# Optimization experiments

Measured on AMD Instinct MI355X. Metric: run time of the kernel, lower is better.

Reference implementation:

```python
import jax, jax.numpy as jnp
import numpy as np

T, C, O, N = 131072, 512, 512, 1024


def setup_inputs() -> dict:
    key = jax.random.key(0)
    k1, k2, k3, k4, k5 = jax.random.split(key, 5)
    x = jax.random.normal(k1, (T, C), dtype=jnp.float32)
    segment_ids = jnp.sort(jax.random.randint(k2, (T,), 0, N)).astype(jnp.int64)
    # proj_func: Linear(C, O); score_func: Linear(C, 1)
    Wp = jax.random.normal(k3, (C, O), dtype=jnp.float32) / np.sqrt(C)
    bp = jnp.zeros((O,), dtype=jnp.float32)
    ws = jax.random.normal(k4, (C,), dtype=jnp.float32) / np.sqrt(C)
    bs = jnp.zeros((), dtype=jnp.float32)
    return {"x": x, "Wp": Wp, "bp": bp, "ws": ws, "bs": bs,
            "segment_ids": segment_ids, "num_segments": N}


def reference(x, Wp, bp, ws, bs, segment_ids, num_segments):
    # proj_x = Linear(x): [T, O]
    proj_x = x @ Wp + bp
    # score = Linear(x) squeezed to [T]
    score = x @ ws + bs
    # segment-wise numerically stable softmax over ragged segments
    seg_max = jax.ops.segment_max(score, segment_ids, num_segments=num_segments)
    seg_max = jnp.where(jnp.isfinite(seg_max), seg_max, 0.0)  # empty segments
    e = jnp.exp(score - seg_max[segment_ids])
    denom = jax.ops.segment_sum(e, segment_ids, num_segments=num_segments)
    w = e / denom[segment_ids]  # [T]
    # per-segment weighted sum of projected features -> [N, O]
    out = jax.ops.segment_sum(proj_x * w[:, None], segment_ids,
                              num_segments=num_segments)
    return out
```

## Files before the change

### kernel.cpp

```cpp
#include <hip/hip_runtime.h>
#include <hip/hip_bf16.h>
#include <cstdint>
#include <cstddef>

#define CC 512
#define OO 512
#define NN 1024
#define QP 4

typedef float f4 __attribute__((ext_vector_type(4)));

__global__ void seg_bounds_kernel(const int* __restrict__ sid,
                                  int* __restrict__ seg_start,
                                  int T, int N) {
    int t = blockIdx.x * blockDim.x + threadIdx.x;
    if (t >= T) return;
    int s  = sid[t];
    int sp = (t == 0) ? -1 : sid[t - 1];
    for (int n = sp + 1; n <= s; ++n) seg_start[n] = t;
    if (t == T - 1) {
        for (int n = s + 1; n <= N; ++n) seg_start[n] = T;
    }
}

__device__ __forceinline__ float dot4(const f4 a, const f4 b) {
    return a.x * b.x + a.y * b.y + a.z * b.z + a.w * b.w;
}

__device__ __forceinline__ float wave_sum(float p) {
    #pragma unroll
    for (int off = 32; off >= 1; off >>= 1)
        p += __shfl_xor(p, off, 64);
    return p;
}

__global__ __launch_bounds__(64) void seg_pool_partial(
    const float* __restrict__ x,
    const float* __restrict__ ws_g,
    const float* __restrict__ bs_g,
    const int*   __restrict__ seg_start,
    float*       __restrict__ pacc,
    float*       __restrict__ pl)
{
    const int g = blockIdx.x;
    const int n = g >> 2;
    const int q = g & 3;
    const int s = seg_start[n];
    const int e = seg_start[n + 1];
    const int len = e - s;
    const int tb = s + (((len * q) >> 2) & ~7);
    const int te = (q == 3) ? e : (s + (((len * (q + 1)) >> 2) & ~7));
    const int lane = threadIdx.x;
    const int c0 = lane * 4;

    const f4 w0 = *reinterpret_cast<const f4*>(ws_g + c0);
    const f4 w1 = *reinterpret_cast<const f4*>(ws_g + 256 + c0);
    const float bsv = bs_g[0];

    float l = 0.f;
    f4 a0 = {0.f, 0.f, 0.f, 0.f};
    f4 a1 = {0.f, 0.f, 0.f, 0.f};

    const int nCh   = (te - tb) >> 2;
    const int start = ((g & 7) * nCh) >> 3;

    f4 A0[4], A1[4], B0[4], B1[4];

    auto PTR = [&](int i) {
        int idx = start + i;
        idx = (idx >= nCh) ? (idx - nCh) : idx;
        return x + (size_t)(tb + idx * 4) * CC;
    };

    auto LOAD4 = [&](f4 (&b0)[4], f4 (&b1)[4], const float* p) {
        #pragma unroll
        for (int j = 0; j < 4; ++j) {
            const float* r = p + (size_t)j * CC;
            b0[j] = __builtin_nontemporal_load(reinterpret_cast<const f4*>(r + c0));
            b1[j] = __builtin_nontemporal_load(reinterpret_cast<const f4*>(r + 256 + c0));
        }
    };

    auto COMP4 = [&](const f4 (&b0)[4], const f4 (&b1)[4]) {
        float sc[4];
        #pragma unroll
        for (int j = 0; j < 4; ++j)
            sc[j] = wave_sum(dot4(b0[j], w0) + dot4(b1[j], w1)) + bsv;
        #pragma unroll
        for (int j = 0; j < 4; ++j) {
            const float wj = __expf(sc[j]);
            l += wj;
            a0 += wj * b0[j];
            a1 += wj * b1[j];
        }
    };

    if (nCh > 0) {
        LOAD4(A0, A1, PTR(0));
        int i = 0;
        for (; i + 1 < nCh; i += 2) {
            LOAD4(B0, B1, PTR(i + 1));
            COMP4(A0, A1);
            if (i + 2 < nCh) LOAD4(A0, A1, PTR(i + 2));
            COMP4(B0, B1);
        }
        if (nCh & 1) COMP4(A0, A1);
    }

    for (int t0 = tb + nCh * 4; t0 < te; t0 += 4) {
        #pragma unroll
        for (int j = 0; j < 4; ++j) {
            int t = t0 + j;
            t = (t < te) ? t : (te - 1);
            const float* r = x + (size_t)t * CC;
            A0[j] = __builtin_nontemporal_load(reinterpret_cast<const f4*>(r + c0));
            A1[j] = __builtin_nontemporal_load(reinterpret_cast<const f4*>(r + 256 + c0));
        }
        #pragma unroll
        for (int j = 0; j < 4; ++j) {
            float sc = wave_sum(dot4(A0[j], w0) + dot4(A1[j], w1)) + bsv;
            if (t0 + j >= te) sc = -INFINITY;
            const float wj = __expf(sc);
            l += wj;
            a0 += wj * A0[j];
            a1 += wj * A1[j];
        }
    }

    float* pa = pacc + (size_t)g * CC;
    *reinterpret_cast<f4*>(pa + c0)       = a0;
    *reinterpret_cast<f4*>(pa + 256 + c0) = a1;
    if (lane == 0) pl[g] = l;
}

__global__ __launch_bounds__(64) void seg_combine(
    const float* __restrict__ pacc,
    const float* __restrict__ pl,
    float*       __restrict__ y)
{
    const int n = blockIdx.x;
    const int lane = threadIdx.x;
    const int c0 = lane * 4;

    float L = 0.f;
    f4 o0 = {0.f, 0.f, 0.f, 0.f};
    f4 o1 = {0.f, 0.f, 0.f, 0.f};
    #pragma unroll
    for (int q = 0; q < QP; ++q) {
        L += pl[n * QP + q];
        const float* pa = pacc + (size_t)(n * QP + q) * CC;
        o0 += *reinterpret_cast<const f4*>(pa + c0);
        o1 += *reinterpret_cast<const f4*>(pa + 256 + c0);
    }
    const float inv = (L > 0.f) ? (1.f / L) : 0.f;
    o0 *= inv;
    o1 *= inv;
    float* yp = y + (size_t)n * CC;
    *reinterpret_cast<f4*>(yp + c0)       = o0;
    *reinterpret_cast<f4*>(yp + 256 + c0) = o1;
}

__global__ __launch_bounds__(256) void proj_kernel(
    float*       __restrict__ out,
    const float* __restrict__ Wp,
    const float* __restrict__ bp,
    const int*   __restrict__ seg_start)
{
    const int n0  = blockIdx.x * 4;
    const int tid = threadIdx.x;

    __shared__ float ylds[4][CC];
    {
        const float* src = out + (size_t)n0 * CC;
        for (int idx = tid; idx < 4 * CC / 4; idx += 256)
            reinterpret_cast<f4*>(&ylds[0][0])[idx] =
                reinterpret_cast<const f4*>(src)[idx];
    }
    __syncthreads();

    const int o0 = tid;
    const int o1 = tid + 256;
    float acc[4][2] = {};

    for (int k = 0; k < CC; k += 4) {
        f4 yv[4];
        #pragma unroll
        for (int r = 0; r < 4; ++r)
            yv[r] = *reinterpret_cast<const f4*>(&ylds[r][k]);
        #pragma unroll
        for (int kk = 0; kk < 4; ++kk) {
            const float w0 = Wp[(size_t)(k + kk) * OO + o0];
            const float w1 = Wp[(size_t)(k + kk) * OO + o1];
            #pragma unroll
            for (int r = 0; r < 4; ++r) {
                const float yval = (kk == 0) ? yv[r].x :
                                   (kk == 1) ? yv[r].y :
                                   (kk == 2) ? yv[r].z : yv[r].w;
                acc[r][0] += yval * w0;
                acc[r][1] += yval * w1;
            }
        }
    }

    #pragma unroll
    for (int r = 0; r < 4; ++r) {
        const int n = n0 + r;
        const bool nonempty = seg_start[n + 1] > seg_start[n];
        const float b0 = nonempty ? bp[o0] : 0.f;
        const float b1 = nonempty ? bp[o1] : 0.f;
        out[(size_t)n * OO + o0] = acc[r][0] + b0;
        out[(size_t)n * OO + o1] = acc[r][1] + b1;
    }
}

extern "C" void kernel_launch(void* const* d_in, const int* in_sizes, int n_in,
                              void* d_out, int out_size, void* d_ws, size_t ws_size,
                              hipStream_t stream) {
    const float* x    = (const float*)d_in[0];
    const float* Wp   = (const float*)d_in[1];
    const float* bp   = (const float*)d_in[2];
    const float* wsv  = (const float*)d_in[3];
    const float* bs   = (const float*)d_in[4];
    const int*   sid  = (const int*)d_in[5];
    const int T = in_sizes[5];
    const int N = NN;

    int*   seg_start = (int*)d_ws;
    float* pacc      = (float*)((char*)d_ws + 8192);
    float* pl        = (float*)((char*)d_ws + 8192 +
                                (size_t)N * QP * CC * sizeof(float));
    float* out       = (float*)d_out;

    seg_bounds_kernel<<<(T + 255) / 256, 256, 0, stream>>>(sid, seg_start, T, N);
    seg_pool_partial<<<N * QP, 64, 0, stream>>>(x, wsv, bs, seg_start, pacc, pl);
    seg_combine<<<N, 64, 0, stream>>>(pacc, pl, out);
    proj_kernel<<<N / 4, 256, 0, stream>>>(out, Wp, bp, seg_start);
}
```

Before: 89.25 us.

## Fuse partial combine into projection GEMM and simplify pooling pipeline

Merges the separate combine kernel into the projection kernel: each 512-thread block sums the four partial accumulators for 8 segments into LDS, applies the 1/L normalisation after the matmul, and writes the output directly. This drops one launch and the intermediate write and read of the pooled features. The pooling loop is restructured into sequential 8-row A/B double buffering, the rotated start offset is removed, and nontemporal loads become plain loads. The projection tile also changes from 4 segments x 2 outputs per thread to 8 segments x 1 output per thread. Possible costs are lower occupancy from 512-thread blocks and fewer blocks (128) in the projection stage.

```diff
diff --git a/kernel.cpp b/kernel.cpp
--- a/kernel.cpp
+++ b/kernel.cpp
@@ -7,6 +7,7 @@
 #define OO 512
 #define NN 1024
 #define QP 4
+#define RB 8
 
 typedef float f4 __attribute__((ext_vector_type(4)));
 
@@ -61,60 +62,78 @@
     f4 a0 = {0.f, 0.f, 0.f, 0.f};
     f4 a1 = {0.f, 0.f, 0.f, 0.f};
 
-    const int nCh   = (te - tb) >> 2;
-    const int start = ((g & 7) * nCh) >> 3;
+    const int nPair = (te - tb) >> 3;
 
     f4 A0[4], A1[4], B0[4], B1[4];
 
-    auto PTR = [&](int i) {
-        int idx = start + i;
-        idx = (idx >= nCh) ? (idx - nCh) : idx;
-        return x + (size_t)(tb + idx * 4) * CC;
-    };
-
-    auto LOAD4 = [&](f4 (&b0)[4], f4 (&b1)[4], const float* p) {
+    auto LOAD4A = [&](const float* p) {
         #pragma unroll
         for (int j = 0; j < 4; ++j) {
             const float* r = p + (size_t)j * CC;
-            b0[j] = __builtin_nontemporal_load(reinterpret_cast<const f4*>(r + c0));
-            b1[j] = __builtin_nontemporal_load(reinterpret_cast<const f4*>(r + 256 + c0));
-        }
-    };
-
-    auto COMP4 = [&](const f4 (&b0)[4], const f4 (&b1)[4]) {
+            A0[j] = *reinterpret_cast<const f4*>(r + c0);
+            A1[j] = *reinterpret_cast<const f4*>(r + 256 + c0);
+        }
+    };
+    auto LOAD4B = [&](const float* p) {
+        #pragma unroll
+        for (int j = 0; j < 4; ++j) {
+            const float* r = p + (size_t)j * CC;
+            B0[j] = *reinterpret_cast<const f4*>(r + c0);
+            B1[j] = *reinterpret_cast<const f4*>(r + 256 + c0);
+        }
+    };
+
+    auto COMP4A = [&]() {
         float sc[4];
         #pragma unroll
         for (int j = 0; j < 4; ++j)
-            sc[j] = wave_sum(dot4(b0[j], w0) + dot4(b1[j], w1)) + bsv;
+            sc[j] = wave_sum(dot4(A0[j], w0) + dot4(A1[j], w1)) + bsv;
         #pragma unroll
         for (int j = 0; j < 4; ++j) {
             const float wj = __expf(sc[j]);
             l += wj;
-            a0 += wj * b0[j];
-            a1 += wj * b1[j];
-        }
-    };
-
-    if (nCh > 0) {
-        LOAD4(A0, A1, PTR(0));
-        int i = 0;
-        for (; i + 1 < nCh; i += 2) {
-            LOAD4(B0, B1, PTR(i + 1));
-            COMP4(A0, A1);
-            if (i + 2 < nCh) LOAD4(A0, A1, PTR(i + 2));
-            COMP4(B0, B1);
-        }
-        if (nCh & 1) COMP4(A0, A1);
-    }
-
-    for (int t0 = tb + nCh * 4; t0 < te; t0 += 4) {
+            a0 += wj * A0[j];
+            a1 += wj * A1[j];
+        }
+    };
+    auto COMP4B = [&]() {
+        float sc[4];
+        #pragma unroll
+        for (int j = 0; j < 4; ++j)
+            sc[j] = wave_sum(dot4(B0[j], w0) + dot4(B1[j], w1)) + bsv;
+        #pragma unroll
+        for (int j = 0; j < 4; ++j) {
+            const float wj = __expf(sc[j]);
+            l += wj;
+            a0 += wj * B0[j];
+            a1 += wj * B1[j];
+        }
+    };
+
+    const float* base = x + (size_t)tb * CC;
+
+    if (nPair >= 1) {
+        LOAD4A(base);
+        LOAD4B(base + 4 * CC);
+        for (int p = 0; p < nPair - 1; ++p) {
+            const float* nxt = base + (size_t)(p * 8 + 8) * CC;
+            COMP4A();
+            LOAD4A(nxt);
+            COMP4B();
+            LOAD4B(nxt + 4 * CC);
+        }
+        COMP4A();
+        COMP4B();
+    }
+
+    for (int t0 = tb + nPair * 8; t0 < te; t0 += 4) {
         #pragma unroll
         for (int j = 0; j < 4; ++j) {
             int t = t0 + j;
             t = (t < te) ? t : (te - 1);
             const float* r = x + (size_t)t * CC;
-            A0[j] = __builtin_nontemporal_load(reinterpret_cast<const f4*>(r + c0));
-            A1[j] = __builtin_nontemporal_load(reinterpret_cast<const f4*>(r + 256 + c0));
+            A0[j] = *reinterpret_cast<const f4*>(r + c0);
+            A1[j] = *reinterpret_cast<const f4*>(r + 256 + c0);
         }
         #pragma unroll
         for (int j = 0; j < 4; ++j) {
@@ -133,83 +152,58 @@
     if (lane == 0) pl[g] = l;
 }
 
-__global__ __launch_bounds__(64) void seg_combine(
+__global__ __launch_bounds__(512) void proj_combine(
     const float* __restrict__ pacc,
     const float* __restrict__ pl,
-    float*       __restrict__ y)
-{
-    const int n = blockIdx.x;
-    const int lane = threadIdx.x;
-    const int c0 = lane * 4;
-
-    float L = 0.f;
-    f4 o0 = {0.f, 0.f, 0.f, 0.f};
-    f4 o1 = {0.f, 0.f, 0.f, 0.f};
-    #pragma unroll
-    for (int q = 0; q < QP; ++q) {
-        L += pl[n * QP + q];
-        const float* pa = pacc + (size_t)(n * QP + q) * CC;
-        o0 += *reinterpret_cast<const f4*>(pa + c0);
-        o1 += *reinterpret_cast<const f4*>(pa + 256 + c0);
-    }
-    const float inv = (L > 0.f) ? (1.f / L) : 0.f;
-    o0 *= inv;
-    o1 *= inv;
-    float* yp = y + (size_t)n * CC;
-    *reinterpret_cast<f4*>(yp + c0)       = o0;
-    *reinterpret_cast<f4*>(yp + 256 + c0) = o1;
-}
-
-__global__ __launch_bounds__(256) void proj_kernel(
-    float*       __restrict__ out,
     const float* __restrict__ Wp,
     const float* __restrict__ bp,
-    const int*   __restrict__ seg_start)
+    float*       __restrict__ out)
 {
-    const int n0  = blockIdx.x * 4;
+    const int n0  = blockIdx.x * RB;
     const int tid = threadIdx.x;
 
-    __shared__ float ylds[4][CC];
-    {
-        const float* src = out + (size_t)n0 * CC;
-        for (int idx = tid; idx < 4 * CC / 4; idx += 256)
-            reinterpret_cast<f4*>(&ylds[0][0])[idx] =
-                reinterpret_cast<const f4*>(src)[idx];
+    __shared__ float ylds[RB][CC];
+    __shared__ float lsh[RB];
+
+    for (int idx = tid; idx < RB * CC / 4; idx += 512) {
+        const int r  = idx >> 7;
+        const int c4 = idx & 127;
+        f4 v = {0.f, 0.f, 0.f, 0.f};
+        #pragma unroll
+        for (int qq = 0; qq < QP; ++qq)
+            v += *reinterpret_cast<const f4*>(
+                     pacc + (size_t)((n0 + r) * QP + qq) * CC + c4 * 4);
+        *reinterpret_cast<f4*>(&ylds[r][c4 * 4]) = v;
+    }
+    if (tid < RB) {
+        float L = 0.f;
+        #pragma unroll
+        for (int qq = 0; qq < QP; ++qq) L += pl[(n0 + tid) * QP + qq];
+        lsh[tid] = (L > 0.f) ? (1.f / L) : 0.f;
     }
     __syncthreads();
 
-    const int o0 = tid;
-    const int o1 = tid + 256;
-    float acc[4][2] = {};
+    const int o = tid;
+    float acc[RB] = {};
 
     for (int k = 0; k < CC; k += 4) {
-        f4 yv[4];
-        #pragma unroll
-        for (int r = 0; r < 4; ++r)
-            yv[r] = *reinterpret_cast<const f4*>(&ylds[r][k]);
-        #pragma unroll
-        for (int kk = 0; kk < 4; ++kk) {
-            const float w0 = Wp[(size_t)(k + kk) * OO + o0];
-            const float w1 = Wp[(size_t)(k + kk) * OO + o1];
-            #pragma unroll
-            for (int r = 0; r < 4; ++r) {
-                const float yval = (kk == 0) ? yv[r].x :
-                                   (kk == 1) ? yv[r].y :
-                                   (kk == 2) ? yv[r].z : yv[r].w;
-                acc[r][0] += yval * w0;
-                acc[r][1] += yval * w1;
-            }
-        }
-    }
-
+        float wv[4];
+        #pragma unroll
+        for (int kk = 0; kk < 4; ++kk)
+            wv[kk] = Wp[(size_t)(k + kk) * OO + o];
+        #pragma unroll
+        for (int r = 0; r < RB; ++r) {
+            const f4 y = *reinterpret_cast<const f4*>(&ylds[r][k]);
+            acc[r] += y.x * wv[0] + y.y * wv[1] + y.z * wv[2] + y.w * wv[3];
+        }
+    }
+
+    const float bv = bp[o];
     #pragma unroll
-    for (int r = 0; r < 4; ++r) {
-        const int n = n0 + r;
-        const bool nonempty = seg_start[n + 1] > seg_start[n];
-        const float b0 = nonempty ? bp[o0] : 0.f;
-        const float b1 = nonempty ? bp[o1] : 0.f;
-        out[(size_t)n * OO + o0] = acc[r][0] + b0;
-        out[(size_t)n * OO + o1] = acc[r][1] + b1;
+    for (int r = 0; r < RB; ++r) {
+        const float linv = lsh[r];
+        const float bias = (linv > 0.f) ? bv : 0.f;
+        out[(size_t)(n0 + r) * OO + o] = acc[r] * linv + bias;
     }
 }
 
@@ -233,6 +227,5 @@
 
     seg_bounds_kernel<<<(T + 255) / 256, 256, 0, stream>>>(sid, seg_start, T, N);
     seg_pool_partial<<<N * QP, 64, 0, stream>>>(x, wsv, bs, seg_start, pacc, pl);
-    seg_combine<<<N, 64, 0, stream>>>(pacc, pl, out);
-    proj_kernel<<<N / 4, 256, 0, stream>>>(out, Wp, bp, seg_start);
-}
+    proj_combine<<<N / RB, 512, 0, stream>>>(pacc, pl, Wp, bp, out);
+}
```

Measured after the change: 112.0 us. +25.4%, slower.

## Fuse segment partial pooling and combine into one block with LDS reduction

Applied to the files above, without the earlier changes.

Replaces the four separate one-wave blocks per segment plus a separate combine kernel with a single 256-thread block per segment. Its four waves interleave 4-row chunks of the segment and reduce their partial sums through shared memory. This removes the partial-accumulator round trip through global memory and one kernel launch. In exchange it loses the rotated start offsets that spread concurrent reads, and it changes the interleaving from contiguous quarters to strided chunks.

```diff
diff --git a/kernel.cpp b/kernel.cpp
--- a/kernel.cpp
+++ b/kernel.cpp
@@ -6,7 +6,6 @@
 #define CC 512
 #define OO 512
 #define NN 1024
-#define QP 4
 
 typedef float f4 __attribute__((ext_vector_type(4)));
 
@@ -34,24 +33,23 @@
     return p;
 }
 
-__global__ __launch_bounds__(64) void seg_pool_partial(
+__global__ __launch_bounds__(256) void seg_pool_block(
     const float* __restrict__ x,
     const float* __restrict__ ws_g,
     const float* __restrict__ bs_g,
     const int*   __restrict__ seg_start,
-    float*       __restrict__ pacc,
-    float*       __restrict__ pl)
+    float*       __restrict__ y)
 {
-    const int g = blockIdx.x;
-    const int n = g >> 2;
-    const int q = g & 3;
-    const int s = seg_start[n];
-    const int e = seg_start[n + 1];
+    const int n    = blockIdx.x;
+    const int q    = threadIdx.x >> 6;
+    const int lane = threadIdx.x & 63;
+    const int c0   = lane * 4;
+
+    const int s   = seg_start[n];
+    const int e   = seg_start[n + 1];
     const int len = e - s;
-    const int tb = s + (((len * q) >> 2) & ~7);
-    const int te = (q == 3) ? e : (s + (((len * (q + 1)) >> 2) & ~7));
-    const int lane = threadIdx.x;
-    const int c0 = lane * 4;
+    const int nFull = len >> 2;
+    const int rag   = len & 3;
 
     const f4 w0 = *reinterpret_cast<const f4*>(ws_g + c0);
     const f4 w1 = *reinterpret_cast<const f4*>(ws_g + 256 + c0);
@@ -61,15 +59,12 @@
     f4 a0 = {0.f, 0.f, 0.f, 0.f};
     f4 a1 = {0.f, 0.f, 0.f, 0.f};
 
-    const int nCh   = (te - tb) >> 2;
-    const int start = ((g & 7) * nCh) >> 3;
+    const int nIt = (nFull > q) ? ((nFull - q + 3) >> 2) : 0;
 
     f4 A0[4], A1[4], B0[4], B1[4];
 
     auto PTR = [&](int i) {
-        int idx = start + i;
-        idx = (idx >= nCh) ? (idx - nCh) : idx;
-        return x + (size_t)(tb + idx * 4) * CC;
+        return x + (size_t)(s + 4 * q + 16 * i) * CC;
     };
 
     auto LOAD4 = [&](f4 (&b0)[4], f4 (&b1)[4], const float* p) {
@@ -95,23 +90,24 @@
         }
     };
 
-    if (nCh > 0) {
+    if (nIt > 0) {
         LOAD4(A0, A1, PTR(0));
         int i = 0;
-        for (; i + 1 < nCh; i += 2) {
+        for (; i + 1 < nIt; i += 2) {
             LOAD4(B0, B1, PTR(i + 1));
             COMP4(A0, A1);
-            if (i + 2 < nCh) LOAD4(A0, A1, PTR(i + 2));
+            if (i + 2 < nIt) LOAD4(A0, A1, PTR(i + 2));
             COMP4(B0, B1);
         }
-        if (nCh & 1) COMP4(A0, A1);
-    }
-
-    for (int t0 = tb + nCh * 4; t0 < te; t0 += 4) {
+        if (nIt & 1) COMP4(A0, A1);
+    }
+
+    if (rag != 0 && q == (nFull & 3)) {
+        const int t0 = s + 4 * nFull;
         #pragma unroll
         for (int j = 0; j < 4; ++j) {
             int t = t0 + j;
-            t = (t < te) ? t : (te - 1);
+            t = (t < e) ? t : (e - 1);
             const float* r = x + (size_t)t * CC;
             A0[j] = __builtin_nontemporal_load(reinterpret_cast<const f4*>(r + c0));
             A1[j] = __builtin_nontemporal_load(reinterpret_cast<const f4*>(r + 256 + c0));
@@ -119,7 +115,7 @@
         #pragma unroll
         for (int j = 0; j < 4; ++j) {
             float sc = wave_sum(dot4(A0[j], w0) + dot4(A1[j], w1)) + bsv;
-            if (t0 + j >= te) sc = -INFINITY;
+            if (t0 + j >= e) sc = -INFINITY;
             const float wj = __expf(sc);
             l += wj;
             a0 += wj * A0[j];
@@ -127,37 +123,24 @@
         }
     }
 
-    float* pa = pacc + (size_t)g * CC;
-    *reinterpret_cast<f4*>(pa + c0)       = a0;
-    *reinterpret_cast<f4*>(pa + 256 + c0) = a1;
-    if (lane == 0) pl[g] = l;
-}
-
-__global__ __launch_bounds__(64) void seg_combine(
-    const float* __restrict__ pacc,
-    const float* __restrict__ pl,
-    float*       __restrict__ y)
-{
-    const int n = blockIdx.x;
-    const int lane = threadIdx.x;
-    const int c0 = lane * 4;
-
-    float L = 0.f;
-    f4 o0 = {0.f, 0.f, 0.f, 0.f};
-    f4 o1 = {0.f, 0.f, 0.f, 0.f};
-    #pragma unroll
-    for (int q = 0; q < QP; ++q) {
-        L += pl[n * QP + q];
-        const float* pa = pacc + (size_t)(n * QP + q) * CC;
-        o0 += *reinterpret_cast<const f4*>(pa + c0);
-        o1 += *reinterpret_cast<const f4*>(pa + 256 + c0);
-    }
-    const float inv = (L > 0.f) ? (1.f / L) : 0.f;
-    o0 *= inv;
-    o1 *= inv;
-    float* yp = y + (size_t)n * CC;
-    *reinterpret_cast<f4*>(yp + c0)       = o0;
-    *reinterpret_cast<f4*>(yp + 256 + c0) = o1;
+    __shared__ float lsa[4][CC];
+    __shared__ float lsl[4];
+    *reinterpret_cast<f4*>(&lsa[q][c0])       = a0;
+    *reinterpret_cast<f4*>(&lsa[q][256 + c0]) = a1;
+    if (lane == 0) lsl[q] = l;
+    __syncthreads();
+
+    if (threadIdx.x < 128) {
+        const int c4 = threadIdx.x * 4;
+        f4 v = *reinterpret_cast<const f4*>(&lsa[0][c4]);
+        v += *reinterpret_cast<const f4*>(&lsa[1][c4]);
+        v += *reinterpret_cast<const f4*>(&lsa[2][c4]);
+        v += *reinterpret_cast<const f4*>(&lsa[3][c4]);
+        const float L = lsl[0] + lsl[1] + lsl[2] + lsl[3];
+        const float inv = (L > 0.f) ? (1.f / L) : 0.f;
+        v *= inv;
+        *reinterpret_cast<f4*>(y + (size_t)n * CC + c4) = v;
+    }
 }
 
 __global__ __launch_bounds__(256) void proj_kernel(
@@ -226,13 +209,9 @@
     const int N = NN;
 
     int*   seg_start = (int*)d_ws;
-    float* pacc      = (float*)((char*)d_ws + 8192);
-    float* pl        = (float*)((char*)d_ws + 8192 +
-                                (size_t)N * QP * CC * sizeof(float));
     float* out       = (float*)d_out;
 
     seg_bounds_kernel<<<(T + 255) / 256, 256, 0, stream>>>(sid, seg_start, T, N);
-    seg_pool_partial<<<N * QP, 64, 0, stream>>>(x, wsv, bs, seg_start, pacc, pl);
-    seg_combine<<<N, 64, 0, stream>>>(pacc, pl, out);
+    seg_pool_block<<<N, 256, 0, stream>>>(x, wsv, bs, seg_start, out);
     proj_kernel<<<N / 4, 256, 0, stream>>>(out, Wp, bp, seg_start);
 }
```

Result: faster. 76.09 us, median of 2 (-14.7%).
